# Optimization experiments

Hardware: AMD Instinct MI355X
Metric: run time of the kernel (lower is better)

Reference implementation:

```python
import jax, jax.numpy as jnp
import numpy as np

B, T, C = 1, 2048, 1024
H = 16
D = C // H
FF = 4 * C


def layernorm(x, g, b, eps=1e-5):
    mu = jnp.mean(x, axis=-1, keepdims=True)
    var = jnp.var(x, axis=-1, keepdims=True)
    return (x - mu) * jax.lax.rsqrt(var + eps) * g + b


def setup_inputs() -> dict:
    key = jax.random.key(0)
    ks = jax.random.split(key, 16)
    s = 0.02
    return {
        "x": jax.random.normal(ks[0], (B, T, C), jnp.float32),
        "qkv_w": jax.random.normal(ks[1], (C, 3 * C), jnp.float32) * s,
        "qkv_b": jnp.zeros((3 * C,), jnp.float32),
        "out_w": jax.random.normal(ks[2], (C, C), jnp.float32) * s,
        "out_b": jnp.zeros((C,), jnp.float32),
        "ln1_g": jnp.ones((C,), jnp.float32),
        "ln1_b": jnp.zeros((C,), jnp.float32),
        "ln2_g": jnp.ones((C,), jnp.float32),
        "ln2_b": jnp.zeros((C,), jnp.float32),
        "w1": jax.random.normal(ks[3], (C, FF), jnp.float32) * s,
        "b1": jnp.zeros((FF,), jnp.float32),
        "w2": jax.random.normal(ks[4], (FF, C), jnp.float32) * s,
        "b2": jnp.zeros((C,), jnp.float32),
    }


def linear_attention(h, qkv_w, qkv_b, out_w, out_b):
    qkv = h @ qkv_w + qkv_b                      # (B,T,3C)
    q, k, v = jnp.split(qkv, 3, axis=-1)
    # (B,T,C) -> (B,H,T,D)
    reshape = lambda a: a.reshape(B, T, H, D).transpose(0, 2, 1, 3)
    q, k, v = reshape(q), reshape(k), reshape(v)
    Q = jax.nn.elu(q) + 1.0
    K = jax.nn.elu(k) + 1.0
    # causal linear attention via cumulative outer-products
    KV = jnp.einsum('bhtd,bhte->bhtde', K, v)    # (B,H,T,D,D)
    KV_cum = jnp.cumsum(KV, axis=2)
    K_cum = jnp.cumsum(K, axis=2)
    num = jnp.einsum('bhtd,bhtde->bhte', Q, KV_cum)
    den = jnp.einsum('bhtd,bhtd->bht', Q, K_cum)[..., None]
    o = num / (den + 1e-6)                       # (B,H,T,D)
    o = o.transpose(0, 2, 1, 3).reshape(B, T, C)
    return o @ out_w + out_b


def reference(x, qkv_w, qkv_b, out_w, out_b, ln1_g, ln1_b, ln2_g, ln2_b, w1, b1, w2, b2):
    x = x + linear_attention(layernorm(x, ln1_g, ln1_b), qkv_w, qkv_b, out_w, out_b)
    h = layernorm(x, ln2_g, ln2_b)
    mlp = jax.nn.gelu(h @ w1 + b1, approximate=False) @ w2 + b2
    return x + mlp
```

## Files before the change

kernel.cpp:

```cpp
#include <hip/hip_runtime.h>

typedef unsigned short u16;
typedef __bf16 bf16x8 __attribute__((ext_vector_type(8)));
typedef float f32x4 __attribute__((ext_vector_type(4)));
typedef unsigned short u16x8 __attribute__((ext_vector_type(8)));
typedef unsigned short u16x4 __attribute__((ext_vector_type(4)));

__device__ __forceinline__ float bf2f(u16 u){
  union { unsigned i; float f; } v; v.i = ((unsigned)u) << 16; return v.f;
}
__device__ __forceinline__ u16 f2bf(float f){
  union { float f; unsigned i; } v; v.f = f;
  unsigned r = v.i + 0x7FFFu + ((v.i >> 16) & 1u);
  return (u16)(r >> 16);
}
__device__ __forceinline__ float elup(float x){ return x > 0.f ? x + 1.f : expf(x); }

__device__ __forceinline__ void gload_lds16(const void* gsrc, void* ldst){
  __builtin_amdgcn_global_load_lds(
      (__attribute__((address_space(1))) void*)(unsigned long long)gsrc,
      (__attribute__((address_space(3))) void*)(unsigned)(unsigned long long)ldst,
      16, 0, 0);
}

struct TD { const float* in; u16* out; int R, Cc, cx, ntiles; };

__global__ __launch_bounds__(256) void transpose4(TD d0, TD d1, TD d2, TD d3){
  __shared__ u16 tile[32][33];
  int b = blockIdx.x;
  TD d;
  if (b < d0.ntiles) d = d0;
  else { b -= d0.ntiles;
    if (b < d1.ntiles) d = d1;
    else { b -= d1.ntiles;
      if (b < d2.ntiles) d = d2;
      else { b -= d2.ntiles; d = d3; } } }
  int c0 = (b % d.cx) * 32, r0 = (b / d.cx) * 32;
  int tx = threadIdx.x, ty = threadIdx.y;
  #pragma unroll
  for (int i=0;i<4;i++)
    tile[ty + i*8][tx] = f2bf(d.in[(size_t)(r0 + ty + i*8)*d.Cc + c0 + tx]);
  __syncthreads();
  #pragma unroll
  for (int i=0;i<4;i++)
    d.out[(size_t)(c0 + ty + i*8)*d.R + r0 + tx] = tile[tx][ty + i*8];
}

__global__ __launch_bounds__(256) void ln_f32(const float* __restrict__ x, const float* __restrict__ g,
                                              const float* __restrict__ b, u16* __restrict__ y){
  int row = blockIdx.x, tid = threadIdx.x;
  size_t base = (size_t)row*1024 + tid*4;
  f32x4 xv = *(const f32x4*)(x + base);
  float v0=xv[0], v1=xv[1], v2=xv[2], v3=xv[3];
  float s  = v0+v1+v2+v3;
  float s2 = v0*v0+v1*v1+v2*v2+v3*v3;
  #pragma unroll
  for (int off=32; off>0; off>>=1){ s += __shfl_xor(s, off); s2 += __shfl_xor(s2, off); }
  __shared__ float ls[4], ls2[4];
  if ((tid & 63) == 0){ ls[tid>>6] = s; ls2[tid>>6] = s2; }
  __syncthreads();
  float ts = ls[0]+ls[1]+ls[2]+ls[3];
  float ts2 = ls2[0]+ls2[1]+ls2[2]+ls2[3];
  float mean = ts*(1.f/1024.f);
  float var  = ts2*(1.f/1024.f) - mean*mean;
  float rstd = rsqrtf(var + 1e-5f);
  f32x4 gv = *(const f32x4*)(g + tid*4);
  f32x4 bv = *(const f32x4*)(b + tid*4);
  u16x4 ov;
  ov[0]=f2bf((v0-mean)*rstd*gv[0]+bv[0]);
  ov[1]=f2bf((v1-mean)*rstd*gv[1]+bv[1]);
  ov[2]=f2bf((v2-mean)*rstd*gv[2]+bv[2]);
  ov[3]=f2bf((v3-mean)*rstd*gv[3]+bv[3]);
  *(u16x4*)(y + base) = ov;
}

template<int EPI>
__global__ __launch_bounds__(256) void gemm_bt(const u16* __restrict__ A, const u16* __restrict__ BT,
                                               const float* __restrict__ bias, const float* __restrict__ res,
                                               void* __restrict__ out, int N, int K, size_t pstride){
  __shared__ u16 As[2][128*32];
  __shared__ u16 Bs[2][128*32];
  int tid = threadIdx.x;
  int w = tid >> 6, lane = tid & 63;
  int m0 = blockIdx.x * 128, n0 = blockIdx.y * 128;
  int Kc = K / gridDim.z;
  int kbase = blockIdx.z * Kc;
  int nt = Kc / 32;

  f32x4 acc[4][4] = {};

  const u16* aSrc = A  + (size_t)(m0 + w*32 + (lane>>2))*K + kbase + (lane&3)*8;
  const u16* bSrc = BT + (size_t)(n0 + w*32 + (lane>>2))*K + kbase + (lane&3)*8;
  int r0 = (w>>1)*64, c0 = (w&1)*64;
  int lrow = lane & 15, lk = (lane>>4)*8;

  {
    u16* aD = As[0] + w*1024;
    u16* bD = Bs[0] + w*1024;
    gload_lds16(aSrc,                aD);
    gload_lds16(aSrc + (size_t)16*K, aD + 512);
    gload_lds16(bSrc,                bD);
    gload_lds16(bSrc + (size_t)16*K, bD + 512);
  }
  __syncthreads();

  int cur = 0;
  for (int t = 0; t < nt; ++t){
    if (t + 1 < nt){
      int k0 = (t+1)*32;
      u16* aD = As[cur^1] + w*1024;
      u16* bD = Bs[cur^1] + w*1024;
      gload_lds16(aSrc + k0,                aD);
      gload_lds16(aSrc + (size_t)16*K + k0, aD + 512);
      gload_lds16(bSrc + k0,                bD);
      gload_lds16(bSrc + (size_t)16*K + k0, bD + 512);
    }
    const u16* Ab = As[cur];
    const u16* Bb = Bs[cur];
    bf16x8 af[4], bfv[4];
    #pragma unroll
    for (int mi=0;mi<4;mi++) af[mi]  = *(const bf16x8*)(Ab + (r0 + mi*16 + lrow)*32 + lk);
    #pragma unroll
    for (int ni=0;ni<4;ni++) bfv[ni] = *(const bf16x8*)(Bb + (c0 + ni*16 + lrow)*32 + lk);
    #pragma unroll
    for (int mi=0;mi<4;mi++)
      #pragma unroll
      for (int ni=0;ni<4;ni++)
        acc[mi][ni] = __builtin_amdgcn_mfma_f32_16x16x32_bf16(af[mi], bfv[ni], acc[mi][ni], 0, 0, 0);
    __syncthreads();
    cur ^= 1;
  }

  int lgr = lane >> 4;
  u16* pout = (EPI == 3) ? ((u16*)out + (size_t)blockIdx.z * pstride) : (u16*)out;
  #pragma unroll
  for (int mi=0;mi<4;mi++){
    #pragma unroll
    for (int j=0;j<4;j++){
      int row = m0 + r0 + mi*16 + lgr*4 + j;
      #pragma unroll
      for (int ni=0;ni<4;ni++){
        int col = n0 + c0 + ni*16 + lrow;
        size_t idx = (size_t)row*N + col;
        if constexpr (EPI == 3){
          pout[idx] = f2bf(acc[mi][ni][j]);
        } else {
          float v = acc[mi][ni][j] + bias[col];
          if constexpr (EPI == 0){
            ((u16*)out)[idx] = f2bf(v);
          } else if constexpr (EPI == 1){
            v = 0.5f * v * (1.f + erff(v * 0.70710678118654752f));
            ((u16*)out)[idx] = f2bf(v);
          } else {
            ((float*)out)[idx] = v + res[idx];
          }
        }
      }
    }
  }
}

__global__ __launch_bounds__(256) void reduce2(const u16* __restrict__ P0, const u16* __restrict__ P1,
                                               const float* __restrict__ bias, const float* __restrict__ res,
                                               float* __restrict__ out){
  size_t i = ((size_t)blockIdx.x*256 + threadIdx.x)*4;
  u16x4 a = *(const u16x4*)(P0 + i);
  u16x4 b = *(const u16x4*)(P1 + i);
  f32x4 rv = *(const f32x4*)(res + i);
  f32x4 bv = *(const f32x4*)(bias + (i & 1023));
  f32x4 o;
  #pragma unroll
  for (int j=0;j<4;j++) o[j] = bf2f(a[j]) + bf2f(b[j]) + bv[j] + rv[j];
  *(f32x4*)(out + i) = o;
}

__global__ __launch_bounds__(256) void reduce4(const u16* __restrict__ P0, const u16* __restrict__ P1,
                                               const u16* __restrict__ P2, const u16* __restrict__ P3,
                                               const float* __restrict__ bias, const float* __restrict__ res,
                                               float* __restrict__ out){
  size_t i = ((size_t)blockIdx.x*256 + threadIdx.x)*4;
  u16x4 a = *(const u16x4*)(P0 + i);
  u16x4 b = *(const u16x4*)(P1 + i);
  u16x4 c = *(const u16x4*)(P2 + i);
  u16x4 d = *(const u16x4*)(P3 + i);
  f32x4 rv = *(const f32x4*)(res + i);
  f32x4 bv = *(const f32x4*)(bias + (i & 1023));
  f32x4 o;
  #pragma unroll
  for (int j=0;j<4;j++) o[j] = (bf2f(a[j]) + bf2f(b[j])) + (bf2f(c[j]) + bf2f(d[j])) + bv[j] + rv[j];
  *(f32x4*)(out + i) = o;
}

__global__ __launch_bounds__(256) void attn_chunksum(const u16* __restrict__ qkv, float* __restrict__ S,
                                                     float* __restrict__ Ks){
  __shared__ u16 KT[64*72];
  __shared__ u16 VT[64*72];
  int c = blockIdx.x, h = blockIdx.y, tid = threadIdx.x;
  int t = tid >> 2, seg = tid & 3, e0 = seg*16;
  size_t rowb = (size_t)(c*64 + t)*3072 + h*64 + e0;
  u16x8 k0 = *(const u16x8*)(qkv + rowb + 1024);
  u16x8 k1 = *(const u16x8*)(qkv + rowb + 1032);
  u16x8 v0 = *(const u16x8*)(qkv + rowb + 2048);
  u16x8 v1 = *(const u16x8*)(qkv + rowb + 2056);
  #pragma unroll
  for (int i=0;i<8;i++){
    KT[(e0 + i)*72 + t]     = f2bf(elup(bf2f(k0[i])));
    KT[(e0 + 8 + i)*72 + t] = f2bf(elup(bf2f(k1[i])));
    VT[(e0 + i)*72 + t]     = v0[i];
    VT[(e0 + 8 + i)*72 + t] = v1[i];
  }
  __syncthreads();

  int w = tid >> 6, lane = tid & 63;
  int lr = lane & 15, lk = (lane>>4)*8, g = lane >> 4, cl = lane & 15;
  bf16x8 av_[2];
  #pragma unroll
  for (int kk=0;kk<2;kk++) av_[kk] = *(const bf16x8*)(VT + (w*16 + lr)*72 + kk*32 + lk);
  f32x4 acc[4] = {};
  #pragma unroll
  for (int di=0;di<4;di++){
    #pragma unroll
    for (int kk=0;kk<2;kk++){
      bf16x8 bk = *(const bf16x8*)(KT + (di*16 + lr)*72 + kk*32 + lk);
      acc[di] = __builtin_amdgcn_mfma_f32_16x16x32_bf16(av_[kk], bk, acc[di], 0, 0, 0);
    }
  }
  size_t base = (size_t)(h*32 + c)*4096;
  #pragma unroll
  for (int di=0;di<4;di++)
    #pragma unroll
    for (int j=0;j<4;j++)
      S[base + (size_t)(w*16 + g*4 + j)*64 + di*16 + cl] = acc[di][j];

  float s = 0.f;
  #pragma unroll
  for (int i=0;i<16;i++) s += bf2f(KT[t*72 + e0 + i]);
  s += __shfl_xor(s, 1); s += __shfl_xor(s, 2);
  if (seg == 0) Ks[(size_t)(h*32 + c)*64 + t] = s;
}

__global__ __launch_bounds__(256) void attn_prefix(float* __restrict__ S, float* __restrict__ Ks){
  int g = blockIdx.x, h = blockIdx.y, tid = threadIdx.x;
  size_t hb = (size_t)h * 32 * 4096;
  int idx = g*256 + tid;
  float run = 0.f;
  for (int c=0; c<32; c++){
    size_t p = hb + (size_t)c*4096 + idx;
    float v = S[p]; S[p] = run; run += v;
  }
  if (g == 0 && tid < 64){
    float r2 = 0.f;
    for (int c=0; c<32; c++){
      size_t p = (size_t)(h*32 + c)*64 + tid;
      float v = Ks[p]; Ks[p] = r2; r2 += v;
    }
  }
}

__global__ __launch_bounds__(256) void attn_out(const u16* __restrict__ qkv, const float* __restrict__ S,
                                                const float* __restrict__ Ks, u16* __restrict__ o){
  __shared__ u16 Qs [64*72];
  __shared__ u16 Ksh[64*72];
  __shared__ u16 VT [64*72];
  __shared__ u16 SpT[64*72];
  __shared__ u16 Am [64*72];
  __shared__ float kp[64], den[64];
  int c = blockIdx.x, h = blockIdx.y, tid = threadIdx.x;
  int t = tid >> 2, seg = tid & 3, e0 = seg*16;

  size_t rowb = (size_t)(c*64 + t)*3072 + h*64 + e0;
  u16x8 q0 = *(const u16x8*)(qkv + rowb);
  u16x8 q1 = *(const u16x8*)(qkv + rowb + 8);
  u16x8 k0 = *(const u16x8*)(qkv + rowb + 1024);
  u16x8 k1 = *(const u16x8*)(qkv + rowb + 1032);
  u16x8 v0 = *(const u16x8*)(qkv + rowb + 2048);
  u16x8 v1 = *(const u16x8*)(qkv + rowb + 2056);
  #pragma unroll
  for (int i=0;i<8;i++){
    Qs [t*72 + e0 + i]     = f2bf(elup(bf2f(q0[i])));
    Qs [t*72 + e0 + 8 + i] = f2bf(elup(bf2f(q1[i])));
    Ksh[t*72 + e0 + i]     = f2bf(elup(bf2f(k0[i])));
    Ksh[t*72 + e0 + 8 + i] = f2bf(elup(bf2f(k1[i])));
    VT [(e0 + i)*72 + t]     = v0[i];
    VT [(e0 + 8 + i)*72 + t] = v1[i];
  }
  size_t sbase = (size_t)(h*32 + c)*4096;
  {
    const f32x4* sp = (const f32x4*)(S + sbase + (size_t)t*64 + e0);
    #pragma unroll
    for (int qd=0;qd<4;qd++){
      f32x4 v = sp[qd];
      #pragma unroll
      for (int j=0;j<4;j++) SpT[t*72 + e0 + qd*4 + j] = f2bf(v[j]);
    }
  }
  if (tid < 64) kp[tid] = Ks[(size_t)(h*32 + c)*64 + tid];
  __syncthreads();

  int w = tid >> 6, lane = tid & 63;
  int lr = lane & 15, lk = (lane>>4)*8, g = lane >> 4, cl = lane & 15;

  bf16x8 aq[2];
  #pragma unroll
  for (int kk=0;kk<2;kk++) aq[kk] = *(const bf16x8*)(Qs + (w*16 + lr)*72 + kk*32 + lk);

  f32x4 acc[4] = {};
  #pragma unroll
  for (int ni=0;ni<4;ni++){
    #pragma unroll
    for (int kk=0;kk<2;kk++){
      bf16x8 bs = *(const bf16x8*)(SpT + (ni*16 + lr)*72 + kk*32 + lk);
      acc[ni] = __builtin_amdgcn_mfma_f32_16x16x32_bf16(aq[kk], bs, acc[ni], 0, 0, 0);
    }
  }
  #pragma unroll
  for (int si=0;si<4;si++){
    f32x4 qk = {};
    #pragma unroll
    for (int kk=0;kk<2;kk++){
      bf16x8 bk = *(const bf16x8*)(Ksh + (si*16 + lr)*72 + kk*32 + lk);
      qk = __builtin_amdgcn_mfma_f32_16x16x32_bf16(aq[kk], bk, qk, 0, 0, 0);
    }
    #pragma unroll
    for (int j=0;j<4;j++){
      int rowt = w*16 + g*4 + j;
      int scol = si*16 + cl;
      Am[rowt*72 + scol] = f2bf((scol <= rowt) ? qk[j] : 0.f);
    }
  }
  __syncthreads();

  {
    float dsum = 0.f;
    #pragma unroll
    for (int i=0;i<16;i++) dsum += bf2f(Am[t*72 + e0 + i]);
    #pragma unroll
    for (int i=0;i<16;i++) dsum += bf2f(Qs[t*72 + e0 + i]) * kp[e0 + i];
    dsum += __shfl_xor(dsum, 1); dsum += __shfl_xor(dsum, 2);
    if (seg == 0) den[t] = dsum;
  }
  {
    bf16x8 aa[2];
    #pragma unroll
    for (int kk=0;kk<2;kk++) aa[kk] = *(const bf16x8*)(Am + (w*16 + lr)*72 + kk*32 + lk);
    #pragma unroll
    for (int ni=0;ni<4;ni++){
      #pragma unroll
      for (int kk=0;kk<2;kk++){
        bf16x8 bv = *(const bf16x8*)(VT + (ni*16 + lr)*72 + kk*32 + lk);
        acc[ni] = __builtin_amdgcn_mfma_f32_16x16x32_bf16(aa[kk], bv, acc[ni], 0, 0, 0);
      }
    }
  }
  __syncthreads();

  #pragma unroll
  for (int j=0;j<4;j++){
    int rowt = w*16 + g*4 + j;
    float inv = 1.f/(den[rowt] + 1e-6f);
    #pragma unroll
    for (int ni=0;ni<4;ni++)
      o[(size_t)(c*64 + rowt)*1024 + h*64 + ni*16 + cl] = f2bf(acc[ni][j]*inv);
  }
}

extern "C" void kernel_launch(void* const* d_in, const int* in_sizes, int n_in,
                              void* d_out, int out_size, void* d_ws, size_t ws_size,
                              hipStream_t stream) {
  (void)in_sizes; (void)n_in; (void)out_size; (void)ws_size;
  const float* x     = (const float*)d_in[0];
  const float* qkv_w = (const float*)d_in[1];
  const float* qkv_b = (const float*)d_in[2];
  const float* out_w = (const float*)d_in[3];
  const float* out_b = (const float*)d_in[4];
  const float* ln1_g = (const float*)d_in[5];
  const float* ln1_b = (const float*)d_in[6];
  const float* ln2_g = (const float*)d_in[7];
  const float* ln2_b = (const float*)d_in[8];
  const float* w1    = (const float*)d_in[9];
  const float* b1    = (const float*)d_in[10];
  const float* w2    = (const float*)d_in[11];
  const float* b2    = (const float*)d_in[12];

  char* ws = (char*)d_ws;
  u16*   wT_qkv = (u16*)  (ws);
  u16*   wT_out = (u16*)  (ws +  6291456);
  u16*   wT_w1  = (u16*)  (ws +  8388608);
  u16*   wT_w2  = (u16*)  (ws + 16777216);
  u16*   h1     = (u16*)  (ws + 25165824);
  u16*   qkv    = (u16*)  (ws + 29360128);
  float* Ssum   = (float*)(ws + 41943040);
  float* ksum   = (float*)(ws + 50331648);
  float* x2     = (float*)(ws + 50462720);
  u16*   h2     = (u16*)  (ws + 58851328);
  u16*   o      = h1;
  u16*   a1     = qkv;
  u16*   Pa0    = (u16*)(ws);
  size_t PaStride = (size_t)(29360128) / 2;
  u16*   Pa1    = (u16*)(ws + 29360128);
  u16*   Pm0    = (u16*)(ws);
  u16*   Pm1    = (u16*)(ws +  4194304);
  u16*   Pm2    = (u16*)(ws +  8388608);
  u16*   Pm3    = (u16*)(ws + 12582912);
  size_t PmStride = 2097152;
  float* outp   = (float*)d_out;

  TD t0{qkv_w, wT_qkv, 1024, 3072,  96, 3072};
  TD t1{out_w, wT_out, 1024, 1024,  32, 1024};
  TD t2{w1,    wT_w1,  1024, 4096, 128, 4096};
  TD t3{w2,    wT_w2,  4096, 1024,  32, 4096};
  transpose4<<<12288, dim3(32,8), 0, stream>>>(t0, t1, t2, t3);

  ln_f32<<<2048, 256, 0, stream>>>(x, ln1_g, ln1_b, h1);
  gemm_bt<0><<<dim3(16, 24, 1), 256, 0, stream>>>(h1, wT_qkv, qkv_b, nullptr, qkv, 3072, 1024, 0);

  attn_chunksum<<<dim3(32, 16), 256, 0, stream>>>(qkv, Ssum, ksum);
  attn_prefix  <<<dim3(16, 16), 256, 0, stream>>>(Ssum, ksum);
  attn_out     <<<dim3(32, 16), 256, 0, stream>>>(qkv, Ssum, ksum, o);

  gemm_bt<3><<<dim3(16, 8, 2), 256, 0, stream>>>(o, wT_out, nullptr, nullptr, Pa0, 1024, 1024, PaStride);
  reduce2<<<2048, 256, 0, stream>>>(Pa0, Pa1, out_b, x, x2);

  ln_f32<<<2048, 256, 0, stream>>>(x2, ln2_g, ln2_b, h2);
  gemm_bt<1><<<dim3(16, 32, 1), 256, 0, stream>>>(h2, wT_w1, b1, nullptr, a1, 4096, 1024, 0);

  gemm_bt<3><<<dim3(16, 8, 4), 256, 0, stream>>>(a1, wT_w2, nullptr, nullptr, Pm0, 1024, 4096, PmStride);
  reduce4<<<2048, 256, 0, stream>>>(Pm0, Pm1, Pm2, Pm3, b2, x2, outp);
}
```

Measured before the change: 146.2 us.

## Fuse out-proj split-K reduce with LayerNorm2 and use 512-thread GEMM blocks

Adds a kernel that sums the split-K partials of the attention output projection, adds bias and residual, writes x2 and applies LayerNorm2 in one pass. This replaces the separate reduce2 and ln_f32 launches and removes one read of x2. The GEMM now runs 8 waves of 512 threads per 128x128 tile, so each wave owns a 32x64 sub-tile and issues one load per operand per stage, which halves per-wave register use. The out-projection split-K goes from 2 to 4 slices, which adds partial-buffer traffic in exchange for more blocks.

```diff
diff --git a/kernel.cpp b/kernel.cpp
--- a/kernel.cpp
+++ b/kernel.cpp
@@ -74,8 +74,45 @@
   *(u16x4*)(y + base) = ov;
 }
 
+__global__ __launch_bounds__(256) void ln2_fused(const u16* __restrict__ P0, const u16* __restrict__ P1,
+                                                 const u16* __restrict__ P2, const u16* __restrict__ P3,
+                                                 const float* __restrict__ bias, const float* __restrict__ xres,
+                                                 const float* __restrict__ g, const float* __restrict__ b,
+                                                 float* __restrict__ x2, u16* __restrict__ h2){
+  int row = blockIdx.x, tid = threadIdx.x;
+  size_t base = (size_t)row*1024 + tid*4;
+  u16x4 a0 = *(const u16x4*)(P0 + base);
+  u16x4 a1 = *(const u16x4*)(P1 + base);
+  u16x4 a2 = *(const u16x4*)(P2 + base);
+  u16x4 a3 = *(const u16x4*)(P3 + base);
+  f32x4 rv = *(const f32x4*)(xres + base);
+  f32x4 bv = *(const f32x4*)(bias + tid*4);
+  f32x4 v;
+  #pragma unroll
+  for (int j=0;j<4;j++) v[j] = (bf2f(a0[j])+bf2f(a1[j])) + (bf2f(a2[j])+bf2f(a3[j])) + bv[j] + rv[j];
+  *(f32x4*)(x2 + base) = v;
+  float s  = v[0]+v[1]+v[2]+v[3];
+  float s2 = v[0]*v[0]+v[1]*v[1]+v[2]*v[2]+v[3]*v[3];
+  #pragma unroll
+  for (int off=32; off>0; off>>=1){ s += __shfl_xor(s, off); s2 += __shfl_xor(s2, off); }
+  __shared__ float ls[4], ls2[4];
+  if ((tid & 63) == 0){ ls[tid>>6] = s; ls2[tid>>6] = s2; }
+  __syncthreads();
+  float ts = ls[0]+ls[1]+ls[2]+ls[3];
+  float ts2 = ls2[0]+ls2[1]+ls2[2]+ls2[3];
+  float mean = ts*(1.f/1024.f);
+  float var  = ts2*(1.f/1024.f) - mean*mean;
+  float rstd = rsqrtf(var + 1e-5f);
+  f32x4 gv = *(const f32x4*)(g + tid*4);
+  f32x4 bb = *(const f32x4*)(b + tid*4);
+  u16x4 ov;
+  #pragma unroll
+  for (int j=0;j<4;j++) ov[j] = f2bf((v[j]-mean)*rstd*gv[j]+bb[j]);
+  *(u16x4*)(h2 + base) = ov;
+}
+
 template<int EPI>
-__global__ __launch_bounds__(256) void gemm_bt(const u16* __restrict__ A, const u16* __restrict__ BT,
+__global__ __launch_bounds__(512) void gemm_bt(const u16* __restrict__ A, const u16* __restrict__ BT,
                                                const float* __restrict__ bias, const float* __restrict__ res,
                                                void* __restrict__ out, int N, int K, size_t pstride){
   __shared__ u16 As[2][128*32];
@@ -87,20 +124,16 @@
   int kbase = blockIdx.z * Kc;
   int nt = Kc / 32;
 
-  f32x4 acc[4][4] = {};
-
-  const u16* aSrc = A  + (size_t)(m0 + w*32 + (lane>>2))*K + kbase + (lane&3)*8;
-  const u16* bSrc = BT + (size_t)(n0 + w*32 + (lane>>2))*K + kbase + (lane&3)*8;
-  int r0 = (w>>1)*64, c0 = (w&1)*64;
+  f32x4 acc[2][4] = {};
+
+  const u16* aSrc = A  + (size_t)(m0 + w*16 + (lane>>2))*K + kbase + (lane&3)*8;
+  const u16* bSrc = BT + (size_t)(n0 + w*16 + (lane>>2))*K + kbase + (lane&3)*8;
+  int r0 = (w>>1)*32, c0 = (w&1)*64;
   int lrow = lane & 15, lk = (lane>>4)*8;
 
   {
-    u16* aD = As[0] + w*1024;
-    u16* bD = Bs[0] + w*1024;
-    gload_lds16(aSrc,                aD);
-    gload_lds16(aSrc + (size_t)16*K, aD + 512);
-    gload_lds16(bSrc,                bD);
-    gload_lds16(bSrc + (size_t)16*K, bD + 512);
+    gload_lds16(aSrc, As[0] + w*512);
+    gload_lds16(bSrc, Bs[0] + w*512);
   }
   __syncthreads();
 
@@ -108,22 +141,18 @@
   for (int t = 0; t < nt; ++t){
     if (t + 1 < nt){
       int k0 = (t+1)*32;
-      u16* aD = As[cur^1] + w*1024;
-      u16* bD = Bs[cur^1] + w*1024;
-      gload_lds16(aSrc + k0,                aD);
-      gload_lds16(aSrc + (size_t)16*K + k0, aD + 512);
-      gload_lds16(bSrc + k0,                bD);
-      gload_lds16(bSrc + (size_t)16*K + k0, bD + 512);
+      gload_lds16(aSrc + k0, As[cur^1] + w*512);
+      gload_lds16(bSrc + k0, Bs[cur^1] + w*512);
     }
     const u16* Ab = As[cur];
     const u16* Bb = Bs[cur];
-    bf16x8 af[4], bfv[4];
-    #pragma unroll
-    for (int mi=0;mi<4;mi++) af[mi]  = *(const bf16x8*)(Ab + (r0 + mi*16 + lrow)*32 + lk);
+    bf16x8 af[2], bfv[4];
+    #pragma unroll
+    for (int mi=0;mi<2;mi++) af[mi]  = *(const bf16x8*)(Ab + (r0 + mi*16 + lrow)*32 + lk);
     #pragma unroll
     for (int ni=0;ni<4;ni++) bfv[ni] = *(const bf16x8*)(Bb + (c0 + ni*16 + lrow)*32 + lk);
     #pragma unroll
-    for (int mi=0;mi<4;mi++)
+    for (int mi=0;mi<2;mi++)
       #pragma unroll
       for (int ni=0;ni<4;ni++)
         acc[mi][ni] = __builtin_amdgcn_mfma_f32_16x16x32_bf16(af[mi], bfv[ni], acc[mi][ni], 0, 0, 0);
@@ -134,7 +163,7 @@
   int lgr = lane >> 4;
   u16* pout = (EPI == 3) ? ((u16*)out + (size_t)blockIdx.z * pstride) : (u16*)out;
   #pragma unroll
-  for (int mi=0;mi<4;mi++){
+  for (int mi=0;mi<2;mi++){
     #pragma unroll
     for (int j=0;j<4;j++){
       int row = m0 + r0 + mi*16 + lgr*4 + j;
@@ -148,30 +177,14 @@
           float v = acc[mi][ni][j] + bias[col];
           if constexpr (EPI == 0){
             ((u16*)out)[idx] = f2bf(v);
-          } else if constexpr (EPI == 1){
+          } else {
             v = 0.5f * v * (1.f + erff(v * 0.70710678118654752f));
             ((u16*)out)[idx] = f2bf(v);
-          } else {
-            ((float*)out)[idx] = v + res[idx];
           }
         }
       }
     }
   }
-}
-
-__global__ __launch_bounds__(256) void reduce2(const u16* __restrict__ P0, const u16* __restrict__ P1,
-                                               const float* __restrict__ bias, const float* __restrict__ res,
-                                               float* __restrict__ out){
-  size_t i = ((size_t)blockIdx.x*256 + threadIdx.x)*4;
-  u16x4 a = *(const u16x4*)(P0 + i);
-  u16x4 b = *(const u16x4*)(P1 + i);
-  f32x4 rv = *(const f32x4*)(res + i);
-  f32x4 bv = *(const f32x4*)(bias + (i & 1023));
-  f32x4 o;
-  #pragma unroll
-  for (int j=0;j<4;j++) o[j] = bf2f(a[j]) + bf2f(b[j]) + bv[j] + rv[j];
-  *(f32x4*)(out + i) = o;
 }
 
 __global__ __launch_bounds__(256) void reduce4(const u16* __restrict__ P0, const u16* __restrict__ P1,
@@ -395,9 +408,8 @@
   u16*   h2     = (u16*)  (ws + 58851328);
   u16*   o      = h1;
   u16*   a1     = qkv;
-  u16*   Pa0    = (u16*)(ws);
-  size_t PaStride = (size_t)(29360128) / 2;
-  u16*   Pa1    = (u16*)(ws + 29360128);
+  u16*   Pa0    = (u16*)(ws + 29360128);
+  size_t PaStride = 2097152;
   u16*   Pm0    = (u16*)(ws);
   u16*   Pm1    = (u16*)(ws +  4194304);
   u16*   Pm2    = (u16*)(ws +  8388608);
@@ -412,18 +424,18 @@
   transpose4<<<12288, dim3(32,8), 0, stream>>>(t0, t1, t2, t3);
 
   ln_f32<<<2048, 256, 0, stream>>>(x, ln1_g, ln1_b, h1);
-  gemm_bt<0><<<dim3(16, 24, 1), 256, 0, stream>>>(h1, wT_qkv, qkv_b, nullptr, qkv, 3072, 1024, 0);
+  gemm_bt<0><<<dim3(16, 24, 1), 512, 0, stream>>>(h1, wT_qkv, qkv_b, nullptr, qkv, 3072, 1024, 0);
 
   attn_chunksum<<<dim3(32, 16), 256, 0, stream>>>(qkv, Ssum, ksum);
   attn_prefix  <<<dim3(16, 16), 256, 0, stream>>>(Ssum, ksum);
   attn_out     <<<dim3(32, 16), 256, 0, stream>>>(qkv, Ssum, ksum, o);
 
-  gemm_bt<3><<<dim3(16, 8, 2), 256, 0, stream>>>(o, wT_out, nullptr, nullptr, Pa0, 1024, 1024, PaStride);
-  reduce2<<<2048, 256, 0, stream>>>(Pa0, Pa1, out_b, x, x2);
-
-  ln_f32<<<2048, 256, 0, stream>>>(x2, ln2_g, ln2_b, h2);
-  gemm_bt<1><<<dim3(16, 32, 1), 256, 0, stream>>>(h2, wT_w1, b1, nullptr, a1, 4096, 1024, 0);
-
-  gemm_bt<3><<<dim3(16, 8, 4), 256, 0, stream>>>(a1, wT_w2, nullptr, nullptr, Pm0, 1024, 4096, PmStride);
+  gemm_bt<3><<<dim3(16, 8, 4), 512, 0, stream>>>(o, wT_out, nullptr, nullptr, Pa0, 1024, 1024, PaStride);
+  ln2_fused<<<2048, 256, 0, stream>>>(Pa0, Pa0 + PaStride, Pa0 + 2*PaStride, Pa0 + 3*PaStride,
+                                      out_b, x, ln2_g, ln2_b, x2, h2);
+
+  gemm_bt<1><<<dim3(16, 32, 1), 512, 0, stream>>>(h2, wT_w1, b1, nullptr, a1, 4096, 1024, 0);
+
+  gemm_bt<3><<<dim3(16, 8, 4), 512, 0, stream>>>(a1, wT_w2, nullptr, nullptr, Pm0, 1024, 4096, PmStride);
   reduce4<<<2048, 256, 0, stream>>>(Pm0, Pm1, Pm2, Pm3, b2, x2, outp);
 }
```

After: 142.7 us. 2.4% less time.
